# Kernel tuning notes

Hardware: AMD Instinct MI355X
Metric: run time of the kernel (lower is better)

The kernel has to match this reference:

```python
import jax, jax.numpy as jnp
import numpy as np

N_NODES = 50000


def gcn_conv(x, W, b, src, dst, n_nodes):
    # Linear transform first (PyG GCNConv): [N, out]
    h = x @ W
    # Add self-loops
    loop = jnp.arange(n_nodes, dtype=src.dtype)
    s = jnp.concatenate([src, loop])
    d = jnp.concatenate([dst, loop])
    # Symmetric normalization: deg counted at destination with unit weights
    deg = jax.ops.segment_sum(jnp.ones_like(d, dtype=h.dtype), d, num_segments=n_nodes)
    dinv = jnp.where(deg > 0, jax.lax.rsqrt(deg), 0.0)
    norm = dinv[s] * dinv[d]  # [E+N]
    # Gather source features, scale, scatter-add to destinations
    msgs = h[s] * norm[:, None]
    out = jax.ops.segment_sum(msgs, d, num_segments=n_nodes)
    return out + b


def setup_inputs() -> dict:
    key = jax.random.key(0)
    k1, k2, k3, k4, k5 = jax.random.split(key, 5)
    in_c, out_c = 512, 128
    x = jax.random.normal(k1, (N_NODES, in_c), dtype=jnp.float32)
    edge_index = jax.random.randint(k2, (2, 800000), 0, N_NODES, dtype=jnp.int64)
    glorot = 1.0 / np.sqrt(in_c)
    W_mu = jax.random.uniform(k3, (in_c, out_c), jnp.float32, -glorot, glorot)
    W_logstd = jax.random.uniform(k4, (in_c, out_c), jnp.float32, -glorot, glorot)
    b_mu = jnp.zeros((out_c,), jnp.float32)
    b_logstd = jnp.zeros((out_c,), jnp.float32)
    return {"x": x, "edge_index": edge_index, "W_mu": W_mu, "b_mu": b_mu,
            "W_logstd": W_logstd, "b_logstd": b_logstd}


def reference(x, edge_index, W_mu, b_mu, W_logstd, b_logstd):
    src, dst = edge_index[0], edge_index[1]
    mu = gcn_conv(x, W_mu, b_mu, src, dst, N_NODES)
    logstd = gcn_conv(x, W_logstd, b_logstd, src, dst, N_NODES)
    return mu, logstd
```

## Files before the change

kernel.cpp:

```cpp
#include <hip/hip_runtime.h>

#define NN 50000
#define NE 800000
#define KC 512
#define OC 256
#define NB_SCAN 196

typedef float f32x4 __attribute__((ext_vector_type(4)));
typedef short bf16x8 __attribute__((ext_vector_type(8)));

__device__ __forceinline__ unsigned f2bf(float f) {
    union { float f; unsigned u; } v; v.f = f;
    return (v.u + 0x7FFFu + ((v.u >> 16) & 1u)) >> 16;
}
__device__ __forceinline__ float bf2f(unsigned short b) {
    union { unsigned u; float f; } v; v.u = ((unsigned)b) << 16;
    return v.f;
}

__global__ __launch_bounds__(256) void count_deg_kernel(const int* __restrict__ ei,
                                                        int* __restrict__ deg) {
    int e = blockIdx.x * 256 + threadIdx.x;
    if (e < NE) atomicAdd(&deg[ei[NE + e]], 1);
}

__global__ __launch_bounds__(256) void scan_part_kernel(const int* __restrict__ deg,
                                                        int* __restrict__ partial) {
    int tid = threadIdx.x;
    int i = blockIdx.x * 256 + tid;
    int v = (i < NN) ? deg[i] : 0;
#pragma unroll
    for (int off = 32; off > 0; off >>= 1) v += __shfl_down(v, off, 64);
    __shared__ int wsum[4];
    if ((tid & 63) == 0) wsum[tid >> 6] = v;
    __syncthreads();
    if (tid == 0) partial[blockIdx.x] = wsum[0] + wsum[1] + wsum[2] + wsum[3];
}

__global__ __launch_bounds__(256) void scan_block_kernel(const int* __restrict__ partial,
                                                         int* __restrict__ blockoff) {
    __shared__ int lds[256];
    int tid = threadIdx.x;
    int v = (tid < NB_SCAN) ? partial[tid] : 0;
    lds[tid] = v;
    __syncthreads();
    for (int off = 1; off < 256; off <<= 1) {
        int t = (tid >= off) ? lds[tid - off] : 0;
        __syncthreads();
        lds[tid] += t;
        __syncthreads();
    }
    if (tid < NB_SCAN) blockoff[tid] = lds[tid] - v;
}

__global__ __launch_bounds__(256) void scan_apply_kernel(const int* __restrict__ deg,
                                                         const int* __restrict__ blockoff,
                                                         int* __restrict__ row_start,
                                                         int* __restrict__ cursor,
                                                         float* __restrict__ dinv) {
    int tid = threadIdx.x;
    int lane = tid & 63;
    int w = tid >> 6;
    int i = blockIdx.x * 256 + tid;
    int d = (i < NN) ? deg[i] : 0;
    int v = d;
#pragma unroll
    for (int off = 1; off < 64; off <<= 1) {
        int t = __shfl_up(v, off, 64);
        if (lane >= off) v += t;
    }
    __shared__ int wsum[4];
    if (lane == 63) wsum[w] = v;
    __syncthreads();
    int wof = 0;
    for (int k = 0; k < w; ++k) wof += wsum[k];
    int excl = blockoff[blockIdx.x] + wof + v - d;
    if (i < NN) {
        row_start[i] = excl;
        cursor[i] = excl;
        dinv[i] = rsqrtf((float)(d + 1));
    }
    if (i == NN - 1) row_start[NN] = excl + d;
}

__global__ __launch_bounds__(256) void scatter_kernel(const int* __restrict__ ei,
                                                      int* __restrict__ cursor,
                                                      int* __restrict__ csr_src) {
    int e = blockIdx.x * 256 + threadIdx.x;
    if (e < NE) {
        int d = ei[NE + e];
        int pos = atomicAdd(&cursor[d], 1);
        csr_src[pos] = ei[e];
    }
}

__global__ __launch_bounds__(256) void convw_kernel(const float* __restrict__ Wmu,
                                                    const float* __restrict__ Wls,
                                                    uint4* __restrict__ Wc) {
    int idx = blockIdx.x * 256 + threadIdx.x;
    int kb = idx >> 10;
    int rem = idx & 1023;
    int wf = rem >> 6;
    int lane = rem & 63;
    int g4 = lane >> 4;
    int i16 = lane & 15;
    int col = (wf >> 2) * 64 + (wf & 3) * 16 + i16;
    int k0 = kb * 32 + g4 * 8;
    const float* Wsrc = (col < 128) ? (Wmu + col) : (Wls + (col - 128));
    unsigned o[4];
#pragma unroll
    for (int p = 0; p < 4; ++p) {
        float lo = Wsrc[(size_t)(k0 + 2 * p) * 128];
        float hi = Wsrc[(size_t)(k0 + 2 * p + 1) * 128];
        o[p] = f2bf(lo) | (f2bf(hi) << 16);
    }
    uint4 v;
    v.x = o[0]; v.y = o[1]; v.z = o[2]; v.w = o[3];
    Wc[idx] = v;
}

__global__ __launch_bounds__(256, 4) void gemm_kernel(const float* __restrict__ x,
                                                      const uint4* __restrict__ Wc,
                                                      const float* __restrict__ dinv,
                                                      unsigned short* __restrict__ hs) {
    __shared__ __align__(16) float Af[2][32 * 128];

    int tid = threadIdx.x;
    int lane = tid & 63;
    int w = tid >> 6;
    int r0 = blockIdx.x * 32;
    int i16 = lane & 15;
    int g4 = lane >> 4;

    const float* srcp[4];
#pragma unroll
    for (int j = 0; j < 4; ++j) {
        int r = w * 8 + j * 2 + (lane >> 5);
        int gr = r0 + r;
        if (gr > NN - 1) gr = NN - 1;
        int cp = (lane & 31) >> 1;
        int mp = (lane & 1) * 4;
        int c = cp ^ (r & 15);
        int m = mp ^ (((r >> 2) & 1) * 4);
        srcp[j] = x + (size_t)gr * KC + c * 8 + m;
    }
    auto dmaA = [&](int buf, int S) {
#pragma unroll
        for (int j = 0; j < 4; ++j) {
            __builtin_amdgcn_global_load_lds(
                (const __attribute__((address_space(1))) void*)(srcp[j] + S * 128),
                (__attribute__((address_space(3))) void*)&Af[buf][(w * 4 + j) * 256], 16, 0, 0);
        }
    };

    auto readA = [&](int buf, int ks, int fr) -> bf16x8 {
        int r = fr * 16 + i16;
        int c = ks * 4 + g4;
        int cc = c ^ (r & 15);
        int mo = ((r >> 2) & 1) * 4;
        const float* p = &Af[buf][r * 128 + cc * 8];
        f32x4 lo = *(const f32x4*)(p + mo);
        f32x4 hi = *(const f32x4*)(p + (mo ^ 4));
        unsigned o0, o1, o2, o3;
        asm("v_cvt_pk_bf16_f32 %0, %1, %2" : "=v"(o0) : "v"(lo.x), "v"(lo.y));
        asm("v_cvt_pk_bf16_f32 %0, %1, %2" : "=v"(o1) : "v"(lo.z), "v"(lo.w));
        asm("v_cvt_pk_bf16_f32 %0, %1, %2" : "=v"(o2) : "v"(hi.x), "v"(hi.y));
        asm("v_cvt_pk_bf16_f32 %0, %1, %2" : "=v"(o3) : "v"(hi.z), "v"(hi.w));
        union { unsigned u[4]; bf16x8 v; } res;
        res.u[0] = o0; res.u[1] = o1; res.u[2] = o2; res.u[3] = o3;
        return res.v;
    };

    const uint4* wbase = Wc + (size_t)(w * 4) * 64 + lane;
    uint4 bb[3][4];
    auto loadB = [&](int dbuf, int kb) {
#pragma unroll
        for (int fc = 0; fc < 4; ++fc) bb[dbuf][fc] = wbase[kb * 1024 + fc * 64];
    };

    f32x4 acc[2][4];
    f32x4 zz = {0.f, 0.f, 0.f, 0.f};
#pragma unroll
    for (int a = 0; a < 2; ++a)
#pragma unroll
        for (int b = 0; b < 4; ++b) acc[a][b] = zz;

    dmaA(0, 0);
    loadB(0, 0);
    loadB(1, 1);
    __syncthreads();

#pragma unroll
    for (int S = 0; S < 4; ++S) {
        if (S < 3) dmaA((S + 1) & 1, S + 1);
#pragma unroll
        for (int ks = 0; ks < 4; ++ks) {
            const int kb = S * 4 + ks;
            if (kb + 2 < 16) loadB((kb + 2) % 3, kb + 2);
            bf16x8 af0 = readA(S & 1, ks, 0);
            bf16x8 af1 = readA(S & 1, ks, 1);
            const int cur = kb % 3;
#pragma unroll
            for (int fc = 0; fc < 4; ++fc) {
                bf16x8 bfrag = *(const bf16x8*)&bb[cur][fc];
                acc[0][fc] = __builtin_amdgcn_mfma_f32_16x16x32_bf16(af0, bfrag, acc[0][fc], 0, 0, 0);
                acc[1][fc] = __builtin_amdgcn_mfma_f32_16x16x32_bf16(af1, bfrag, acc[1][fc], 0, 0, 0);
            }
        }
        if (S < 3) __syncthreads();
    }

#pragma unroll
    for (int fr = 0; fr < 2; ++fr) {
#pragma unroll
        for (int r = 0; r < 4; ++r) {
            int gr = r0 + fr * 16 + g4 * 4 + r;
            if (gr < NN) {
                float dv = dinv[gr];
#pragma unroll
                for (int fc = 0; fc < 4; ++fc) {
                    int col = w * 64 + fc * 16 + i16;
                    hs[(size_t)gr * OC + col] = (unsigned short)f2bf(acc[fr][fc][r] * dv);
                }
            }
        }
    }
}

__global__ __launch_bounds__(256) void aggregate_kernel(const unsigned short* __restrict__ hs,
                                                        const int* __restrict__ row_start,
                                                        const int* __restrict__ csr_src,
                                                        const float* __restrict__ dinv,
                                                        const float* __restrict__ bmu,
                                                        const float* __restrict__ bls,
                                                        float* __restrict__ out) {
    int tid = threadIdx.x;
    int lane = tid & 63;
    int node = blockIdx.x * 4 + (tid >> 6);

    const unsigned short* hrow = hs + lane * 4;
    float acc0, acc1, acc2, acc3;
    {
        ushort4 v = *(const ushort4*)&hrow[(size_t)node * OC];
        acc0 = bf2f(v.x);
        acc1 = bf2f(v.y);
        acc2 = bf2f(v.z);
        acc3 = bf2f(v.w);
    }
    int rs = row_start[node], re = row_start[node + 1];
    int e = rs;
    for (; e + 8 <= re; e += 8) {
        int s[8];
#pragma unroll
        for (int q = 0; q < 8; ++q) s[q] = csr_src[e + q];
        ushort4 v[8];
#pragma unroll
        for (int q = 0; q < 8; ++q) v[q] = *(const ushort4*)&hrow[(size_t)s[q] * OC];
#pragma unroll
        for (int q = 0; q < 8; ++q) {
            acc0 += bf2f(v[q].x);
            acc1 += bf2f(v[q].y);
            acc2 += bf2f(v[q].z);
            acc3 += bf2f(v[q].w);
        }
    }
    if (e + 4 <= re) {
        int s[4];
#pragma unroll
        for (int q = 0; q < 4; ++q) s[q] = csr_src[e + q];
        ushort4 v[4];
#pragma unroll
        for (int q = 0; q < 4; ++q) v[q] = *(const ushort4*)&hrow[(size_t)s[q] * OC];
#pragma unroll
        for (int q = 0; q < 4; ++q) {
            acc0 += bf2f(v[q].x);
            acc1 += bf2f(v[q].y);
            acc2 += bf2f(v[q].z);
            acc3 += bf2f(v[q].w);
        }
        e += 4;
    }
    for (; e < re; ++e) {
        int s0 = csr_src[e];
        ushort4 v0 = *(const ushort4*)&hrow[(size_t)s0 * OC];
        acc0 += bf2f(v0.x);
        acc1 += bf2f(v0.y);
        acc2 += bf2f(v0.z);
        acc3 += bf2f(v0.w);
    }
    float dn = dinv[node];
    if (lane < 32) {
        f32x4 b = *(const f32x4*)&bmu[lane * 4];
        f32x4 r;
        r.x = acc0 * dn + b.x;
        r.y = acc1 * dn + b.y;
        r.z = acc2 * dn + b.z;
        r.w = acc3 * dn + b.w;
        __builtin_nontemporal_store(r, (f32x4*)(out + (size_t)node * 128 + lane * 4));
    } else {
        f32x4 b = *(const f32x4*)&bls[(lane - 32) * 4];
        f32x4 r;
        r.x = acc0 * dn + b.x;
        r.y = acc1 * dn + b.y;
        r.z = acc2 * dn + b.z;
        r.w = acc3 * dn + b.w;
        __builtin_nontemporal_store(
            r, (f32x4*)(out + (size_t)NN * 128 + (size_t)node * 128 + (lane - 32) * 4));
    }
}

extern "C" void kernel_launch(void* const* d_in, const int* in_sizes, int n_in,
                              void* d_out, int out_size, void* d_ws, size_t ws_size,
                              hipStream_t stream) {
    const float* x = (const float*)d_in[0];
    const int* ei = (const int*)d_in[1];
    const float* Wmu = (const float*)d_in[2];
    const float* bmu = (const float*)d_in[3];
    const float* Wls = (const float*)d_in[4];
    const float* bls = (const float*)d_in[5];
    float* out = (float*)d_out;

    char* ws = (char*)d_ws;
    size_t off = 0;
    auto alloc = [&](size_t bytes) {
        void* p = ws + off;
        off += (bytes + 255) & ~(size_t)255;
        return p;
    };
    unsigned short* hs = (unsigned short*)alloc((size_t)NN * OC * sizeof(unsigned short));
    uint4* Wc = (uint4*)alloc((size_t)16384 * 16);
    int* deg = (int*)alloc((size_t)NN * sizeof(int));
    int* row_start = (int*)alloc((size_t)(NN + 1) * sizeof(int));
    int* cursor = (int*)alloc((size_t)NN * sizeof(int));
    int* csr_src = (int*)alloc((size_t)NE * sizeof(int));
    float* dinv = (float*)alloc((size_t)NN * sizeof(float));
    int* partial = (int*)alloc((size_t)NB_SCAN * sizeof(int));
    int* blockoff = (int*)alloc((size_t)NB_SCAN * sizeof(int));

    hipMemsetAsync(deg, 0, (size_t)NN * sizeof(int), stream);

    count_deg_kernel<<<(NE + 255) / 256, 256, 0, stream>>>(ei, deg);
    scan_part_kernel<<<NB_SCAN, 256, 0, stream>>>(deg, partial);
    scan_block_kernel<<<1, 256, 0, stream>>>(partial, blockoff);
    scan_apply_kernel<<<NB_SCAN, 256, 0, stream>>>(deg, blockoff, row_start, cursor, dinv);
    scatter_kernel<<<(NE + 255) / 256, 256, 0, stream>>>(ei, cursor, csr_src);
    convw_kernel<<<64, 256, 0, stream>>>(Wmu, Wls, Wc);
    gemm_kernel<<<(NN + 31) / 32, 256, 0, stream>>>(x, Wc, dinv, hs);
    aggregate_kernel<<<NN / 4, 256, 0, stream>>>(hs, row_start, csr_src, dinv, bmu, bls, out);
}
```

Before: 196.9 us.

## Merge prep kernels and run CSR scatter inside GEMM launch

Folds the weight conversion into the degree-count launch and the single-block scan into scan_apply, where each block recomputes the prefix of the partial sums. The CSR scatter blocks are appended to the GEMM grid, so the atomic scatter can overlap with the matrix multiply. This cuts the launch count from eight to five and removes the serial gaps between launches. In exchange, the scatter blocks are sized for the GEMM's shared memory and launch bounds, which may limit their occupancy, and the scan work is repeated in every block.

```diff
diff --git a/kernel.cpp b/kernel.cpp
--- a/kernel.cpp
+++ b/kernel.cpp
@@ -5,6 +5,8 @@
 #define KC 512
 #define OC 256
 #define NB_SCAN 196
+#define NCB 3125
+#define NGB 1563
 
 typedef float f32x4 __attribute__((ext_vector_type(4)));
 typedef short bf16x8 __attribute__((ext_vector_type(8)));
@@ -18,10 +20,38 @@
     return v.f;
 }
 
-__global__ __launch_bounds__(256) void count_deg_kernel(const int* __restrict__ ei,
-                                                        int* __restrict__ deg) {
-    int e = blockIdx.x * 256 + threadIdx.x;
-    if (e < NE) atomicAdd(&deg[ei[NE + e]], 1);
+__global__ __launch_bounds__(256) void prep0_kernel(const int* __restrict__ ei,
+                                                    int* __restrict__ deg,
+                                                    const float* __restrict__ Wmu,
+                                                    const float* __restrict__ Wls,
+                                                    uint4* __restrict__ Wc) {
+    int bid = blockIdx.x;
+    int tid = threadIdx.x;
+    if (bid < NCB) {
+        int e = bid * 256 + tid;
+        if (e < NE) atomicAdd(&deg[ei[NE + e]], 1);
+    } else {
+        int idx = (bid - NCB) * 256 + tid;
+        int kb = idx >> 10;
+        int rem = idx & 1023;
+        int wf = rem >> 6;
+        int lane = rem & 63;
+        int g4 = lane >> 4;
+        int i16 = lane & 15;
+        int col = (wf >> 2) * 64 + (wf & 3) * 16 + i16;
+        int k0 = kb * 32 + g4 * 8;
+        const float* Wsrc = (col < 128) ? (Wmu + col) : (Wls + (col - 128));
+        unsigned o[4];
+#pragma unroll
+        for (int p = 0; p < 4; ++p) {
+            float lo = Wsrc[(size_t)(k0 + 2 * p) * 128];
+            float hi = Wsrc[(size_t)(k0 + 2 * p + 1) * 128];
+            o[p] = f2bf(lo) | (f2bf(hi) << 16);
+        }
+        uint4 v;
+        v.x = o[0]; v.y = o[1]; v.z = o[2]; v.w = o[3];
+        Wc[idx] = v;
+    }
 }
 
 __global__ __launch_bounds__(256) void scan_part_kernel(const int* __restrict__ deg,
@@ -37,30 +67,28 @@
     if (tid == 0) partial[blockIdx.x] = wsum[0] + wsum[1] + wsum[2] + wsum[3];
 }
 
-__global__ __launch_bounds__(256) void scan_block_kernel(const int* __restrict__ partial,
-                                                         int* __restrict__ blockoff) {
-    __shared__ int lds[256];
-    int tid = threadIdx.x;
-    int v = (tid < NB_SCAN) ? partial[tid] : 0;
-    lds[tid] = v;
-    __syncthreads();
-    for (int off = 1; off < 256; off <<= 1) {
-        int t = (tid >= off) ? lds[tid - off] : 0;
-        __syncthreads();
-        lds[tid] += t;
-        __syncthreads();
-    }
-    if (tid < NB_SCAN) blockoff[tid] = lds[tid] - v;
-}
-
 __global__ __launch_bounds__(256) void scan_apply_kernel(const int* __restrict__ deg,
-                                                         const int* __restrict__ blockoff,
+                                                         const int* __restrict__ partial,
                                                          int* __restrict__ row_start,
                                                          int* __restrict__ cursor,
                                                          float* __restrict__ dinv) {
+    __shared__ int plds[256];
+    __shared__ int wsum[4];
     int tid = threadIdx.x;
     int lane = tid & 63;
     int w = tid >> 6;
+
+    int pv = (tid < NB_SCAN) ? partial[tid] : 0;
+    plds[tid] = pv;
+    __syncthreads();
+    for (int off = 1; off < 256; off <<= 1) {
+        int t = (tid >= off) ? plds[tid - off] : 0;
+        __syncthreads();
+        plds[tid] += t;
+        __syncthreads();
+    }
+    int boff = (blockIdx.x == 0) ? 0 : plds[blockIdx.x - 1];
+
     int i = blockIdx.x * 256 + tid;
     int d = (i < NN) ? deg[i] : 0;
     int v = d;
@@ -69,12 +97,11 @@
         int t = __shfl_up(v, off, 64);
         if (lane >= off) v += t;
     }
-    __shared__ int wsum[4];
     if (lane == 63) wsum[w] = v;
     __syncthreads();
     int wof = 0;
     for (int k = 0; k < w; ++k) wof += wsum[k];
-    int excl = blockoff[blockIdx.x] + wof + v - d;
+    int excl = boff + wof + v - d;
     if (i < NN) {
         row_start[i] = excl;
         cursor[i] = excl;
@@ -83,52 +110,31 @@
     if (i == NN - 1) row_start[NN] = excl + d;
 }
 
-__global__ __launch_bounds__(256) void scatter_kernel(const int* __restrict__ ei,
-                                                      int* __restrict__ cursor,
-                                                      int* __restrict__ csr_src) {
-    int e = blockIdx.x * 256 + threadIdx.x;
-    if (e < NE) {
-        int d = ei[NE + e];
-        int pos = atomicAdd(&cursor[d], 1);
-        csr_src[pos] = ei[e];
-    }
-}
-
-__global__ __launch_bounds__(256) void convw_kernel(const float* __restrict__ Wmu,
-                                                    const float* __restrict__ Wls,
-                                                    uint4* __restrict__ Wc) {
-    int idx = blockIdx.x * 256 + threadIdx.x;
-    int kb = idx >> 10;
-    int rem = idx & 1023;
-    int wf = rem >> 6;
-    int lane = rem & 63;
-    int g4 = lane >> 4;
-    int i16 = lane & 15;
-    int col = (wf >> 2) * 64 + (wf & 3) * 16 + i16;
-    int k0 = kb * 32 + g4 * 8;
-    const float* Wsrc = (col < 128) ? (Wmu + col) : (Wls + (col - 128));
-    unsigned o[4];
-#pragma unroll
-    for (int p = 0; p < 4; ++p) {
-        float lo = Wsrc[(size_t)(k0 + 2 * p) * 128];
-        float hi = Wsrc[(size_t)(k0 + 2 * p + 1) * 128];
-        o[p] = f2bf(lo) | (f2bf(hi) << 16);
-    }
-    uint4 v;
-    v.x = o[0]; v.y = o[1]; v.z = o[2]; v.w = o[3];
-    Wc[idx] = v;
-}
-
-__global__ __launch_bounds__(256, 4) void gemm_kernel(const float* __restrict__ x,
-                                                      const uint4* __restrict__ Wc,
-                                                      const float* __restrict__ dinv,
-                                                      unsigned short* __restrict__ hs) {
+__global__ __launch_bounds__(256, 4) void gemm_scatter_kernel(const float* __restrict__ x,
+                                                              const uint4* __restrict__ Wc,
+                                                              const float* __restrict__ dinv,
+                                                              unsigned short* __restrict__ hs,
+                                                              const int* __restrict__ ei,
+                                                              int* __restrict__ cursor,
+                                                              int* __restrict__ csr_src) {
     __shared__ __align__(16) float Af[2][32 * 128];
 
-    int tid = threadIdx.x;
+    int bid = blockIdx.x;
+    int tid = threadIdx.x;
+
+    if (bid >= NGB) {
+        int e = (bid - NGB) * 256 + tid;
+        if (e < NE) {
+            int d = ei[NE + e];
+            int pos = atomicAdd(&cursor[d], 1);
+            csr_src[pos] = ei[e];
+        }
+        return;
+    }
+
     int lane = tid & 63;
     int w = tid >> 6;
-    int r0 = blockIdx.x * 32;
+    int r0 = bid * 32;
     int i16 = lane & 15;
     int g4 = lane >> 4;
 
@@ -335,16 +341,12 @@
     int* csr_src = (int*)alloc((size_t)NE * sizeof(int));
     float* dinv = (float*)alloc((size_t)NN * sizeof(float));
     int* partial = (int*)alloc((size_t)NB_SCAN * sizeof(int));
-    int* blockoff = (int*)alloc((size_t)NB_SCAN * sizeof(int));
 
     hipMemsetAsync(deg, 0, (size_t)NN * sizeof(int), stream);
 
-    count_deg_kernel<<<(NE + 255) / 256, 256, 0, stream>>>(ei, deg);
+    prep0_kernel<<<NCB + 64, 256, 0, stream>>>(ei, deg, Wmu, Wls, Wc);
     scan_part_kernel<<<NB_SCAN, 256, 0, stream>>>(deg, partial);
-    scan_block_kernel<<<1, 256, 0, stream>>>(partial, blockoff);
-    scan_apply_kernel<<<NB_SCAN, 256, 0, stream>>>(deg, blockoff, row_start, cursor, dinv);
-    scatter_kernel<<<(NE + 255) / 256, 256, 0, stream>>>(ei, cursor, csr_src);
-    convw_kernel<<<64, 256, 0, stream>>>(Wmu, Wls, Wc);
-    gemm_kernel<<<(NN + 31) / 32, 256, 0, stream>>>(x, Wc, dinv, hs);
+    scan_apply_kernel<<<NB_SCAN, 256, 0, stream>>>(deg, partial, row_start, cursor, dinv);
+    gemm_scatter_kernel<<<NGB + NCB, 256, 0, stream>>>(x, Wc, dinv, hs, ei, cursor, csr_src);
     aggregate_kernel<<<NN / 4, 256, 0, stream>>>(hs, row_start, csr_src, dinv, bmu, bls, out);
 }
```

Result: faster. 187.3 us (median of 2 runs) (-4.9%).
